# Kernel tuning notes

Hardware: AMD Instinct MI355X
Metric: run time of the kernel (lower is better)

Reference implementation:

```python
import jax, jax.numpy as jnp
import numpy as np

B, C_IN, C_OUT, H, W_SP = 64, 256, 256, 32, 32
G = H * W_SP  # groups == H*W per module assert


def setup_inputs() -> dict:
    key = jax.random.key(0)
    k1, k2, k3 = jax.random.split(key, 3)
    x = jax.random.normal(k1, (B, C_IN, H, W_SP), dtype=jnp.float32)
    # grouped 1x1 conv == per-group linear: weight [G, C_out, C_in], bias [G, C_out]
    W = jax.random.normal(k2, (G, C_OUT, C_IN), dtype=jnp.float32) * (1.0 / np.sqrt(C_IN))
    b = jax.random.normal(k3, (G, C_OUT), dtype=jnp.float32) * 0.01
    return {"x": x, "W": W, "b": b}


def reference(x, W, b):
    Bn, Cin, Hn, Wn = x.shape
    Gn = Hn * Wn
    # permute(0,2,3,1).reshape(B,-1,1,1): channels-last flatten -> [B, G, C_in]
    xg = jnp.transpose(x, (0, 2, 3, 1)).reshape(Bn, Gn, Cin)
    # block-diagonal batched matmul per spatial position (group)
    out = jnp.einsum("bgi,goi->bgo", xg, W) + b  # [B, G, C_out]
    # view(B,H,W,C_out).permute(0,3,1,2)
    return jnp.transpose(out.reshape(Bn, Hn, Wn, -1), (0, 3, 1, 2))
```

## Files before the change

kernel.cpp:

```cpp
#include <hip/hip_runtime.h>
#include <hip/hip_bf16.h>

typedef __bf16 bf16x8 __attribute__((ext_vector_type(8)));
typedef float f32x4 __attribute__((ext_vector_type(4)));

#define GN    1024
#define BATCH 64
#define CIN   256
#define COUT  256
#define NG    4
#define A_BYTES (BATCH * CIN * 2)
#define WCHUNK  16384

#define G_AS __attribute__((address_space(1)))
#define L_AS __attribute__((address_space(3)))

static __device__ __forceinline__ void gload16(const void* g, void* l) {
  __builtin_amdgcn_global_load_lds((const G_AS void*)g, (L_AS void*)l, 16, 0, 0);
}

static __device__ __forceinline__ ushort f2bf(float f) {
  __hip_bfloat16 h = __float2bfloat16(f);
  return *reinterpret_cast<ushort*>(&h);
}
static __device__ __forceinline__ float bf2f(ushort u) {
  uint v = (uint)u << 16;
  return *reinterpret_cast<float*>(&v);
}

__global__ __launch_bounds__(256) void k_transpose_convert(
    const float* __restrict__ x, ushort* __restrict__ xT)
{
  __shared__ float tile[64][65];
  const int g0 = blockIdx.x * 64;
  const int i0 = blockIdx.y * 64;
  const int b  = blockIdx.z;
  const int t  = threadIdx.x;
  const int a  = t & 15;
  const int r  = t >> 4;
  const int key = (b & 7) << 3;

  const float* xb = x + (size_t)b * CIN * GN;
#pragma unroll
  for (int p = 0; p < 4; ++p) {
    int ii = p * 16 + r;
    float4 v = *reinterpret_cast<const float4*>(
        &xb[(size_t)(i0 + ii) * GN + g0 + a * 4]);
    tile[ii][a * 4 + 0] = v.x;
    tile[ii][a * 4 + 1] = v.y;
    tile[ii][a * 4 + 2] = v.z;
    tile[ii][a * 4 + 3] = v.w;
  }
  __syncthreads();

  ushort* xTb = xT + (size_t)b * GN * CIN;
#pragma unroll
  for (int p = 0; p < 4; ++p) {
    int gg = p * 16 + r;
    ushort4 u;
    u.x = f2bf(tile[a * 4 + 0][gg]);
    u.y = f2bf(tile[a * 4 + 1][gg]);
    u.z = f2bf(tile[a * 4 + 2][gg]);
    u.w = f2bf(tile[a * 4 + 3][gg]);
    int isw = (i0 + a * 4) ^ key;
    *reinterpret_cast<ushort4*>(&xTb[(size_t)(g0 + gg) * CIN + isw]) = u;
  }
}

__global__ __launch_bounds__(256) void k_group_gemm(
    const ushort* __restrict__ xT, const float* __restrict__ W,
    const float* __restrict__ bias, float* __restrict__ out,
    ushort* __restrict__ outT, int use_ws)
{
  __shared__ __align__(16) unsigned char lds[A_BYTES + 4 * 2 * WCHUNK];
  ushort* lA        = (ushort*)lds;
  unsigned char* lW = lds + A_BYTES;

  const int tid  = threadIdx.x;
  const int wave = tid >> 6;
  const int lane = tid & 63;
  const int g_base = blockIdx.x * NG;

  const int arow = lane & 15;
  const int q    = lane >> 4;
  const int oc   = 64 * wave + arow;

  unsigned char* lWw = lW + wave * (2 * WCHUNK);

  auto stage_a = [&](int gg) {
#pragma unroll
    for (int j = 0; j < 8; ++j) {
      int b = 16 * wave + 2 * j + (lane >> 5);
      const ushort* gsrc = xT + ((size_t)b * GN + gg) * CIN + (lane & 31) * 8;
      gload16(gsrc, lA + (16 * wave + 2 * j) * CIN);
    }
  };
  auto stage_wc = [&](int sg) {
    const int gg = g_base + (sg >> 2);
    const int c  = sg & 3;
    unsigned char* ldb = lWw + (sg & 1) * WCHUNK;
    const unsigned char* gb = (const unsigned char*)W
        + ((size_t)gg * COUT + 64 * wave + 16 * c) * (CIN * 4);
#pragma unroll
    for (int j = 0; j < 16; ++j) {
      gload16(gb + (size_t)j * (CIN * 4) + ((lane ^ (j & 7)) << 4),
              ldb + j * 1024);
    }
  };

  float bvv[NG][4];
#pragma unroll
  for (int gi = 0; gi < NG; ++gi)
#pragma unroll
    for (int n = 0; n < 4; ++n)
      bvv[gi][n] = bias[(g_base + gi) * COUT + oc + n * 16];
  __builtin_amdgcn_sched_barrier(0);

  stage_a(g_base);
  __builtin_amdgcn_sched_barrier(0);
  stage_wc(0);
  stage_wc(1);
  __builtin_amdgcn_sched_barrier(0);
  asm volatile("s_waitcnt vmcnt(16)" ::: "memory");
  __builtin_amdgcn_sched_barrier(0);
  __builtin_amdgcn_s_barrier();

  const int NTAB[16] = {-1, 16, 16, 16, 32, 32, 16, 16,
                        32, 32, 16, 16, 32, 32, 16, 0};

#pragma unroll
  for (int gi = 0; gi < NG; ++gi) {
    const int g = g_base + gi;

    f32x4 acc[4][4];
#pragma unroll
    for (int m = 0; m < 4; ++m)
#pragma unroll
      for (int n = 0; n < 4; ++n)
        acc[m][n] = {0.f, 0.f, 0.f, 0.f};

#pragma unroll
    for (int c = 0; c < 4; ++c) {
      const int s = gi * 4 + c;
      const int nt = NTAB[s];
      if (nt == 0)       { asm volatile("s_waitcnt vmcnt(0)"  ::: "memory"); }
      else if (nt == 16) { asm volatile("s_waitcnt vmcnt(16)" ::: "memory"); }
      else if (nt == 32) { asm volatile("s_waitcnt vmcnt(32)" ::: "memory"); }
      __builtin_amdgcn_sched_barrier(0);

      unsigned char* wb = lWw + (s & 1) * WCHUNK;
      const int key = (arow & 7) << 4;
      const int rb  = arow * 1024;

#pragma unroll
      for (int ks = 0; ks < 8; ++ks) {
        float4 f0 = *reinterpret_cast<const float4*>(
            wb + rb + ks * 128 + ((q * 32) ^ key));
        float4 f1 = *reinterpret_cast<const float4*>(
            wb + rb + ks * 128 + ((q * 32 + 16) ^ key));

        bf16x8 afr[4];
        const int i0 = ks * 32 + q * 8;
#pragma unroll
        for (int m = 0; m < 4; ++m) {
          int row = m * 16 + arow;
          afr[m] = *reinterpret_cast<const bf16x8*>(
              &lA[row * CIN + (i0 ^ ((row & 7) << 3))]);
        }

        bf16x8 bfr;
        bfr[0] = (__bf16)f0.x; bfr[1] = (__bf16)f0.y;
        bfr[2] = (__bf16)f0.z; bfr[3] = (__bf16)f0.w;
        bfr[4] = (__bf16)f1.x; bfr[5] = (__bf16)f1.y;
        bfr[6] = (__bf16)f1.z; bfr[7] = (__bf16)f1.w;

        __builtin_amdgcn_s_setprio(1);
#pragma unroll
        for (int m = 0; m < 4; ++m)
          acc[m][c] = __builtin_amdgcn_mfma_f32_16x16x32_bf16(
              afr[m], bfr, acc[m][c], 0, 0, 0);
        __builtin_amdgcn_s_setprio(0);
      }

      asm volatile("s_waitcnt lgkmcnt(0)" ::: "memory");
      __builtin_amdgcn_sched_barrier(0);
      if (c < 3) {
        if (s + 2 < 4 * NG) stage_wc(s + 2);
        __builtin_amdgcn_sched_barrier(0);
      }
    }

    __builtin_amdgcn_s_barrier();
    if (gi < NG - 1) stage_a(g + 1);
    {
      const int s = gi * 4 + 3;
      if (s + 2 < 4 * NG) stage_wc(s + 2);
    }
    __builtin_amdgcn_sched_barrier(0);

    if (use_ws) {
#pragma unroll
      for (int m = 0; m < 4; ++m) {
#pragma unroll
        for (int n = 0; n < 4; ++n) {
          int o = oc + n * 16;
          ushort4 u;
          u.x = f2bf(acc[m][n][0] + bvv[gi][n]);
          u.y = f2bf(acc[m][n][1] + bvv[gi][n]);
          u.z = f2bf(acc[m][n][2] + bvv[gi][n]);
          u.w = f2bf(acc[m][n][3] + bvv[gi][n]);
          *reinterpret_cast<ushort4*>(
              &outT[((size_t)g * COUT + o) * BATCH + m * 16 + 4 * q]) = u;
        }
      }
    } else {
#pragma unroll
      for (int m = 0; m < 4; ++m) {
#pragma unroll
        for (int n = 0; n < 4; ++n) {
          int o = oc + n * 16;
#pragma unroll
          for (int j = 0; j < 4; ++j) {
            int b = m * 16 + 4 * q + j;
            out[((size_t)b * COUT + o) * GN + g] = acc[m][n][j] + bvv[gi][n];
          }
        }
      }
    }
    __builtin_amdgcn_sched_barrier(0);
  }
}

__global__ __launch_bounds__(256) void k_transpose_out(
    const ushort* __restrict__ outT, float* __restrict__ out)
{
  __shared__ float tile[64][65];
  const int g0 = blockIdx.x * 64;
  const int o  = blockIdx.y;
  const int t  = threadIdx.x;

  {
    const int a = t & 7;
#pragma unroll
    for (int p = 0; p < 2; ++p) {
      int gl = p * 32 + (t >> 3);
      int4 raw = *reinterpret_cast<const int4*>(
          &outT[((size_t)(g0 + gl) * COUT + o) * BATCH + a * 8]);
      const ushort* us = reinterpret_cast<const ushort*>(&raw);
#pragma unroll
      for (int e = 0; e < 8; ++e) tile[gl][a * 8 + e] = bf2f(us[e]);
    }
  }
  __syncthreads();

  {
    const int a2 = t & 15;
#pragma unroll
    for (int p = 0; p < 4; ++p) {
      int bl = p * 16 + (t >> 4);
      float4 v;
      v.x = tile[4 * a2 + 0][bl];
      v.y = tile[4 * a2 + 1][bl];
      v.z = tile[4 * a2 + 2][bl];
      v.w = tile[4 * a2 + 3][bl];
      *reinterpret_cast<float4*>(
          &out[((size_t)bl * COUT + o) * GN + g0 + 4 * a2]) = v;
    }
  }
}

extern "C" void kernel_launch(void* const* d_in, const int* in_sizes, int n_in,
                              void* d_out, int out_size, void* d_ws, size_t ws_size,
                              hipStream_t stream) {
  const float* x  = (const float*)d_in[0];
  const float* W  = (const float*)d_in[1];
  const float* bs = (const float*)d_in[2];
  float* out      = (float*)d_out;

  const size_t xT_elems = (size_t)BATCH * GN * CIN;
  const size_t oT_elems = (size_t)GN * COUT * BATCH;
  const bool use_ws = ws_size >= (xT_elems + oT_elems) * sizeof(ushort);

  ushort* xT   = (ushort*)d_ws;
  ushort* outT = xT + xT_elems;

  dim3 grid1(GN / 64, CIN / 64, BATCH);
  k_transpose_convert<<<grid1, 256, 0, stream>>>(x, xT);
  k_group_gemm<<<GN / NG, 256, 0, stream>>>(xT, W, bs, out,
                                            use_ws ? outT : nullptr,
                                            use_ws ? 1 : 0);
  if (use_ws) {
    dim3 grid3(GN / 64, COUT);
    k_transpose_out<<<grid3, 256, 0, stream>>>(outT, out);
  }
}
```

Before: 112.8 us.

## Fuse input transpose/convert into grouped GEMM with finer weight streaming

Drops the separate transpose-convert kernel. Each GEMM block now reads its 4 spatial groups of fp32 x directly, converts them to bf16 and writes them into a swizzled LDS buffer that holds all 4 groups, removing the bf16 xT round trip through global memory. Weight staging moves to smaller 4KB slices with one prefetch issued per k-step, and block IDs are remapped across XCDs. The cost is a much larger LDS footprint (single block per CU via launch bounds) and strided 16-byte loads of x from global memory.

```diff
diff --git a/kernel.cpp b/kernel.cpp
--- a/kernel.cpp
+++ b/kernel.cpp
@@ -3,20 +3,27 @@
 
 typedef __bf16 bf16x8 __attribute__((ext_vector_type(8)));
 typedef float f32x4 __attribute__((ext_vector_type(4)));
+typedef unsigned short u16x8 __attribute__((ext_vector_type(8)));
 
 #define GN    1024
 #define BATCH 64
 #define CIN   256
 #define COUT  256
 #define NG    4
-#define A_BYTES (BATCH * CIN * 2)
-#define WCHUNK  16384
+#define A_ELEMS (BATCH * CIN)
+#define WSLICE  4096
 
 #define G_AS __attribute__((address_space(1)))
 #define L_AS __attribute__((address_space(3)))
 
 static __device__ __forceinline__ void gload16(const void* g, void* l) {
   __builtin_amdgcn_global_load_lds((const G_AS void*)g, (L_AS void*)l, 16, 0, 0);
+}
+
+static __device__ __forceinline__ void vmwait(int n) {
+  if (n == 0)       asm volatile("s_waitcnt vmcnt(0)"  ::: "memory");
+  else if (n == 4)  asm volatile("s_waitcnt vmcnt(4)"  ::: "memory");
+  else if (n == 20) asm volatile("s_waitcnt vmcnt(20)" ::: "memory");
 }
 
 static __device__ __forceinline__ ushort f2bf(float f) {
@@ -28,84 +35,39 @@
   return *reinterpret_cast<float*>(&v);
 }
 
-__global__ __launch_bounds__(256) void k_transpose_convert(
-    const float* __restrict__ x, ushort* __restrict__ xT)
-{
-  __shared__ float tile[64][65];
-  const int g0 = blockIdx.x * 64;
-  const int i0 = blockIdx.y * 64;
-  const int b  = blockIdx.z;
-  const int t  = threadIdx.x;
-  const int a  = t & 15;
-  const int r  = t >> 4;
-  const int key = (b & 7) << 3;
-
-  const float* xb = x + (size_t)b * CIN * GN;
-#pragma unroll
-  for (int p = 0; p < 4; ++p) {
-    int ii = p * 16 + r;
-    float4 v = *reinterpret_cast<const float4*>(
-        &xb[(size_t)(i0 + ii) * GN + g0 + a * 4]);
-    tile[ii][a * 4 + 0] = v.x;
-    tile[ii][a * 4 + 1] = v.y;
-    tile[ii][a * 4 + 2] = v.z;
-    tile[ii][a * 4 + 3] = v.w;
-  }
-  __syncthreads();
-
-  ushort* xTb = xT + (size_t)b * GN * CIN;
-#pragma unroll
-  for (int p = 0; p < 4; ++p) {
-    int gg = p * 16 + r;
-    ushort4 u;
-    u.x = f2bf(tile[a * 4 + 0][gg]);
-    u.y = f2bf(tile[a * 4 + 1][gg]);
-    u.z = f2bf(tile[a * 4 + 2][gg]);
-    u.w = f2bf(tile[a * 4 + 3][gg]);
-    int isw = (i0 + a * 4) ^ key;
-    *reinterpret_cast<ushort4*>(&xTb[(size_t)(g0 + gg) * CIN + isw]) = u;
-  }
-}
-
-__global__ __launch_bounds__(256) void k_group_gemm(
-    const ushort* __restrict__ xT, const float* __restrict__ W,
+__global__ __launch_bounds__(256, 1) void k_fused_gemm(
+    const float* __restrict__ x, const float* __restrict__ W,
     const float* __restrict__ bias, float* __restrict__ out,
     ushort* __restrict__ outT, int use_ws)
 {
-  __shared__ __align__(16) unsigned char lds[A_BYTES + 4 * 2 * WCHUNK];
+  __shared__ __align__(16) unsigned char lds[4 * A_ELEMS * 2 + 4 * 2 * WSLICE];
   ushort* lA        = (ushort*)lds;
-  unsigned char* lW = lds + A_BYTES;
+  unsigned char* lW = lds + 4 * A_ELEMS * 2;
 
   const int tid  = threadIdx.x;
   const int wave = tid >> 6;
   const int lane = tid & 63;
-  const int g_base = blockIdx.x * NG;
+
+  const int bid    = blockIdx.x;
+  const int q      = (bid & 7) * 32 + (bid >> 3);
+  const int g_base = q * 4;
 
   const int arow = lane & 15;
-  const int q    = lane >> 4;
+  const int qq   = lane >> 4;
   const int oc   = 64 * wave + arow;
 
-  unsigned char* lWw = lW + wave * (2 * WCHUNK);
-
-  auto stage_a = [&](int gg) {
-#pragma unroll
-    for (int j = 0; j < 8; ++j) {
-      int b = 16 * wave + 2 * j + (lane >> 5);
-      const ushort* gsrc = xT + ((size_t)b * GN + gg) * CIN + (lane & 31) * 8;
-      gload16(gsrc, lA + (16 * wave + 2 * j) * CIN);
-    }
-  };
-  auto stage_wc = [&](int sg) {
-    const int gg = g_base + (sg >> 2);
-    const int c  = sg & 3;
-    unsigned char* ldb = lWw + (sg & 1) * WCHUNK;
-    const unsigned char* gb = (const unsigned char*)W
-        + ((size_t)gg * COUT + 64 * wave + 16 * c) * (CIN * 4);
-#pragma unroll
-    for (int j = 0; j < 16; ++j) {
-      gload16(gb + (size_t)j * (CIN * 4) + ((lane ^ (j & 7)) << 4),
-              ldb + j * 1024);
-    }
+  unsigned char* lWw = lW + wave * (2 * WSLICE);
+  const int swz  = ((lane & 7) ^ ((lane >> 3) & 7)) << 4;
+  const int wrow = lane >> 3;
+
+  auto stage_w = [&](int gg, int oh, int ks, int buf) {
+    unsigned char* ldb = lWw + buf * WSLICE;
+    const unsigned char* gb =
+        (const unsigned char*)(W + ((size_t)gg * COUT + 64 * wave + 32 * oh) * CIN)
+        + ks * 128 + swz;
+#pragma unroll
+    for (int j = 0; j < 4; ++j)
+      gload16(gb + (size_t)(8 * j + wrow) * (CIN * 4), ldb + j * 1024);
   };
 
   float bvv[NG][4];
@@ -114,23 +76,51 @@
 #pragma unroll
     for (int n = 0; n < 4; ++n)
       bvv[gi][n] = bias[(g_base + gi) * COUT + oc + n * 16];
+
+  stage_w(g_base, 0, 0, 0);
+  stage_w(g_base, 0, 1, 1);
   __builtin_amdgcn_sched_barrier(0);
 
-  stage_a(g_base);
-  __builtin_amdgcn_sched_barrier(0);
-  stage_wc(0);
-  stage_wc(1);
-  __builtin_amdgcn_sched_barrier(0);
-  asm volatile("s_waitcnt vmcnt(16)" ::: "memory");
-  __builtin_amdgcn_sched_barrier(0);
-  __builtin_amdgcn_s_barrier();
-
-  const int NTAB[16] = {-1, 16, 16, 16, 32, 32, 16, 16,
-                        32, 32, 16, 16, 32, 32, 16, 0};
+  {
+    const int bl = 16 * wave + 2 * ((lane >> 3) & 7);
+#pragma unroll
+    for (int bb = 0; bb < 2; ++bb) {
+      const int b = bl + bb;
+      const int bswz = (b & 7);
+#pragma unroll
+      for (int jj = 0; jj < 4; ++jj) {
+        const int c = (lane & 7) + 8 * jj;
+        float4 v[8];
+#pragma unroll
+        for (int k = 0; k < 8; ++k)
+          v[k] = *reinterpret_cast<const float4*>(
+              &x[((size_t)b * CIN + 8 * c + k) * GN + g_base]);
+        u16x8 u0, u1, u2, u3;
+#pragma unroll
+        for (int k = 0; k < 8; ++k) {
+          u0[k] = f2bf(v[k].x);
+          u1[k] = f2bf(v[k].y);
+          u2[k] = f2bf(v[k].z);
+          u3[k] = f2bf(v[k].w);
+        }
+        const int slot = (c ^ bswz) * 8;
+        ushort* r0 = lA + 0 * A_ELEMS + b * CIN + slot;
+        ushort* r1 = lA + 1 * A_ELEMS + b * CIN + slot;
+        ushort* r2 = lA + 2 * A_ELEMS + b * CIN + slot;
+        ushort* r3 = lA + 3 * A_ELEMS + b * CIN + slot;
+        *reinterpret_cast<u16x8*>(r0) = u0;
+        *reinterpret_cast<u16x8*>(r1) = u1;
+        *reinterpret_cast<u16x8*>(r2) = u2;
+        *reinterpret_cast<u16x8*>(r3) = u3;
+      }
+    }
+  }
+  __syncthreads();
 
 #pragma unroll
   for (int gi = 0; gi < NG; ++gi) {
     const int g = g_base + gi;
+    const ushort* lAg = lA + gi * A_ELEMS;
 
     f32x4 acc[4][4];
 #pragma unroll
@@ -140,63 +130,61 @@
         acc[m][n] = {0.f, 0.f, 0.f, 0.f};
 
 #pragma unroll
-    for (int c = 0; c < 4; ++c) {
-      const int s = gi * 4 + c;
-      const int nt = NTAB[s];
-      if (nt == 0)       { asm volatile("s_waitcnt vmcnt(0)"  ::: "memory"); }
-      else if (nt == 16) { asm volatile("s_waitcnt vmcnt(16)" ::: "memory"); }
-      else if (nt == 32) { asm volatile("s_waitcnt vmcnt(32)" ::: "memory"); }
-      __builtin_amdgcn_sched_barrier(0);
-
-      unsigned char* wb = lWw + (s & 1) * WCHUNK;
-      const int key = (arow & 7) << 4;
-      const int rb  = arow * 1024;
-
+    for (int oh = 0; oh < 2; ++oh) {
 #pragma unroll
       for (int ks = 0; ks < 8; ++ks) {
-        float4 f0 = *reinterpret_cast<const float4*>(
-            wb + rb + ks * 128 + ((q * 32) ^ key));
-        float4 f1 = *reinterpret_cast<const float4*>(
-            wb + rb + ks * 128 + ((q * 32 + 16) ^ key));
-
+        const int s = gi * 16 + oh * 8 + ks;
+        if (s == 63)                       vmwait(0);
+        else if (gi > 0 && (s & 15) < 2)   vmwait(20);
+        else                               vmwait(4);
+        __builtin_amdgcn_sched_barrier(0);
+
+        unsigned char* wb = lWw + (s & 1) * WSLICE;
+        const int key = (arow & 7) << 4;
+
+        float4 f[2][2];
+#pragma unroll
+        for (int n2 = 0; n2 < 2; ++n2) {
+          int r = n2 * 16 + arow;
+          f[n2][0] = *reinterpret_cast<const float4*>(wb + r * 128 + ((qq * 32) ^ key));
+          f[n2][1] = *reinterpret_cast<const float4*>(wb + r * 128 + ((qq * 32 + 16) ^ key));
+        }
         bf16x8 afr[4];
-        const int i0 = ks * 32 + q * 8;
+        const int i0 = ks * 32 + qq * 8;
 #pragma unroll
         for (int m = 0; m < 4; ++m) {
           int row = m * 16 + arow;
           afr[m] = *reinterpret_cast<const bf16x8*>(
-              &lA[row * CIN + (i0 ^ ((row & 7) << 3))]);
-        }
-
-        bf16x8 bfr;
-        bfr[0] = (__bf16)f0.x; bfr[1] = (__bf16)f0.y;
-        bfr[2] = (__bf16)f0.z; bfr[3] = (__bf16)f0.w;
-        bfr[4] = (__bf16)f1.x; bfr[5] = (__bf16)f1.y;
-        bfr[6] = (__bf16)f1.z; bfr[7] = (__bf16)f1.w;
+              &lAg[row * CIN + (i0 ^ ((row & 7) << 3))]);
+        }
+
+        asm volatile("s_waitcnt lgkmcnt(0)" ::: "memory");
+        __builtin_amdgcn_sched_barrier(0);
+        if (s + 2 < 64) {
+          const int s2 = s + 2;
+          stage_w(g_base + (s2 >> 4), (s2 >> 3) & 1, s2 & 7, s2 & 1);
+        }
+        __builtin_amdgcn_sched_barrier(0);
+
+        bf16x8 bfr[2];
+#pragma unroll
+        for (int n2 = 0; n2 < 2; ++n2) {
+          bfr[n2][0] = (__bf16)f[n2][0].x; bfr[n2][1] = (__bf16)f[n2][0].y;
+          bfr[n2][2] = (__bf16)f[n2][0].z; bfr[n2][3] = (__bf16)f[n2][0].w;
+          bfr[n2][4] = (__bf16)f[n2][1].x; bfr[n2][5] = (__bf16)f[n2][1].y;
+          bfr[n2][6] = (__bf16)f[n2][1].z; bfr[n2][7] = (__bf16)f[n2][1].w;
+        }
 
         __builtin_amdgcn_s_setprio(1);
 #pragma unroll
         for (int m = 0; m < 4; ++m)
-          acc[m][c] = __builtin_amdgcn_mfma_f32_16x16x32_bf16(
-              afr[m], bfr, acc[m][c], 0, 0, 0);
+#pragma unroll
+          for (int n2 = 0; n2 < 2; ++n2)
+            acc[m][2 * oh + n2] = __builtin_amdgcn_mfma_f32_16x16x32_bf16(
+                afr[m], bfr[n2], acc[m][2 * oh + n2], 0, 0, 0);
         __builtin_amdgcn_s_setprio(0);
       }
-
-      asm volatile("s_waitcnt lgkmcnt(0)" ::: "memory");
-      __builtin_amdgcn_sched_barrier(0);
-      if (c < 3) {
-        if (s + 2 < 4 * NG) stage_wc(s + 2);
-        __builtin_amdgcn_sched_barrier(0);
-      }
-    }
-
-    __builtin_amdgcn_s_barrier();
-    if (gi < NG - 1) stage_a(g + 1);
-    {
-      const int s = gi * 4 + 3;
-      if (s + 2 < 4 * NG) stage_wc(s + 2);
-    }
-    __builtin_amdgcn_sched_barrier(0);
+    }
 
     if (use_ws) {
 #pragma unroll
@@ -210,7 +198,7 @@
           u.z = f2bf(acc[m][n][2] + bvv[gi][n]);
           u.w = f2bf(acc[m][n][3] + bvv[gi][n]);
           *reinterpret_cast<ushort4*>(
-              &outT[((size_t)g * COUT + o) * BATCH + m * 16 + 4 * q]) = u;
+              &outT[((size_t)g * COUT + o) * BATCH + m * 16 + 4 * qq]) = u;
         }
       }
     } else {
@@ -221,7 +209,7 @@
           int o = oc + n * 16;
 #pragma unroll
           for (int j = 0; j < 4; ++j) {
-            int b = m * 16 + 4 * q + j;
+            int b = m * 16 + 4 * qq + j;
             out[((size_t)b * COUT + o) * GN + g] = acc[m][n][j] + bvv[gi][n];
           }
         }
@@ -277,16 +265,12 @@
   const float* bs = (const float*)d_in[2];
   float* out      = (float*)d_out;
 
-  const size_t xT_elems = (size_t)BATCH * GN * CIN;
   const size_t oT_elems = (size_t)GN * COUT * BATCH;
-  const bool use_ws = ws_size >= (xT_elems + oT_elems) * sizeof(ushort);
-
-  ushort* xT   = (ushort*)d_ws;
-  ushort* outT = xT + xT_elems;
-
-  dim3 grid1(GN / 64, CIN / 64, BATCH);
-  k_transpose_convert<<<grid1, 256, 0, stream>>>(x, xT);
-  k_group_gemm<<<GN / NG, 256, 0, stream>>>(xT, W, bs, out,
+  const bool use_ws = ws_size >= oT_elems * sizeof(ushort);
+
+  ushort* outT = (ushort*)d_ws;
+
+  k_fused_gemm<<<GN / NG, 256, 0, stream>>>(x, W, bs, out,
                                             use_ws ? outT : nullptr,
                                             use_ws ? 1 : 0);
   if (use_ws) {
```

Result: slower. 128.0 us (+13.5%).
